# Kernel optimization log

Hardware: AMD Instinct MI355X
Metric: run time of the kernel (lower is better)

## Reference

```python
import jax, jax.numpy as jnp
import numpy as np

B = 256      # number of graphs
IN = 128     # input_dim
FD = 256     # feature_dim (dims[1])
HID = 256    # hidden_dim of attention block (dims[2])
OUT = 128    # final output dim (dims[3])
TXT = 512    # text_emb_dim

LENGTHS = np.asarray(128 + (np.arange(B) % 256), dtype=np.int64)  # ragged lens 128..383
N = int(LENGTHS.sum())  # 65408 total nodes
LMAX = int(LENGTHS.max())  # 383


def setup_inputs() -> dict:
    key = jax.random.key(0)
    ks = jax.random.split(key, 16)
    s = 0.02
    return {
        "input": jax.random.normal(ks[0], (N, IN), jnp.float32),
        "text_emb": jax.random.normal(ks[1], (B, TXT), jnp.float32),
        "repeat_list": jnp.asarray(LENGTHS),
        # layer 0: Linear(IN -> FD)
        "W0": jax.random.normal(ks[2], (IN, FD), jnp.float32) * s,
        "b0": jax.random.normal(ks[3], (FD,), jnp.float32) * s,
        # cross-attention block params
        "Wq": jax.random.normal(ks[4], (TXT, FD), jnp.float32) * s,
        "bq": jax.random.normal(ks[5], (FD,), jnp.float32) * s,
        "Wk": jax.random.normal(ks[6], (FD, FD), jnp.float32) * s,
        "bk": jax.random.normal(ks[7], (FD,), jnp.float32) * s,
        "Wv": jax.random.normal(ks[8], (FD, FD), jnp.float32) * s,
        "bv": jax.random.normal(ks[9], (FD,), jnp.float32) * s,
        "Wo": jax.random.normal(ks[10], (FD, HID), jnp.float32) * s,
        "bo": jax.random.normal(ks[11], (HID,), jnp.float32) * s,
        # layer 2: Linear(HID -> OUT), last layer (no activation)
        "W2": jax.random.normal(ks[12], (HID, OUT), jnp.float32) * s,
        "b2": jax.random.normal(ks[13], (OUT,), jnp.float32) * s,
    }


def _cross_attention(h, text_emb, repeat_list, Wq, bq, Wk, bk, Wv, bv, Wo, bo):
    # h: [N, FD] packed ragged node features; repeat_list: [B] lengths (constant ints)
    n = h.shape[0]
    b = repeat_list.shape[0]
    fd = h.shape[1]
    # pad ragged -> [B, LMAX, FD] (pad value 0) + validity mask
    seg = jnp.repeat(jnp.arange(b), repeat_list, total_repeat_length=n)  # [N] graph id
    offsets = jnp.cumsum(repeat_list) - repeat_list                      # [B] start of each graph
    pos = jnp.arange(n) - offsets[seg]                                   # [N] within-graph pos
    padded = jnp.zeros((b, LMAX, fd), h.dtype).at[seg, pos].set(h)
    valid = jnp.arange(LMAX)[None, :] < repeat_list[:, None]             # [B, L]

    q = text_emb @ Wq + bq                              # [B, FD]
    k = (padded @ Wk + bk) * valid[..., None]           # masked_fill(mask==0, 0)
    v = (padded @ Wv + bv) * valid[..., None]

    # query is broadcast identically over the padded-length axis, so each row of the
    # [L, L] score matrix is the same vector: scores[b, j] = q[b] . k[b, j]
    scores = jnp.einsum('bf,bjf->bj', q, k)             # [B, L]
    scores = jnp.where(valid, scores, -jnp.inf)         # mask invalid columns j
    p = jax.nn.softmax(scores, axis=-1)                 # [B, L]
    # output = attention^T @ value with identical rows => out[b,j,:] = p[b,j] * sum_i v[b,i,:]
    v_sum = v.sum(axis=1)                               # [B, FD] (padded rows already zero)
    out_pad = p[..., None] * v_sum[:, None, :]          # [B, L, FD]
    out_nodes = out_pad[seg, pos]                       # unpad-concat -> [N, FD]
    return out_nodes @ Wo + bo                          # [N, HID]


def reference(input, text_emb, repeat_list, W0, b0, Wq, bq, Wk, bk, Wv, bv, Wo, bo, W2, b2):
    h = jax.nn.relu(input @ W0 + b0)                                     # layer 0 + relu
    h = _cross_attention(h, text_emb, repeat_list, Wq, bq, Wk, bk, Wv, bv, Wo, bo)
    h = jax.nn.relu(h)                                                   # layer 1 + relu
    return h @ W2 + b2                                                   # layer 2 (last, no act)
```

## Files before the change

### kernel.cpp

```cpp
#include <hip/hip_runtime.h>
#include <math.h>

#define B_G   256
#define IN_D  128
#define FD    256
#define HID   256
#define OUT_D 128
#define TXT   512
#define XKS   136

typedef short bf16x8 __attribute__((ext_vector_type(8)));
typedef float f32x4  __attribute__((ext_vector_type(4)));

__device__ __forceinline__ unsigned bf_rne(float x) {
    unsigned u = __float_as_uint(x);
    u += 0x7fffu + ((u >> 16) & 1u);
    return u >> 16;
}
__device__ __forceinline__ float bf_to_f(unsigned h) {
    return __uint_as_float(h << 16);
}
__device__ __forceinline__ void split2(float a0, float a1, unsigned& hp, unsigned& lp) {
    unsigned h0 = bf_rne(a0), h1 = bf_rne(a1);
    float r0 = a0 - bf_to_f(h0), r1 = a1 - bf_to_f(h1);
    hp = h0 | (h1 << 16);
    lp = bf_rne(r0) | (bf_rne(r1) << 16);
}

__global__ __launch_bounds__(256) void k_prepA(
    const float* __restrict__ text_emb, const float* __restrict__ Wq,
    const float* __restrict__ bq, const float* __restrict__ Wk,
    const float* __restrict__ W0, const int* __restrict__ lens,
    float* __restrict__ qk, int* __restrict__ offsets, float* __restrict__ hsum,
    unsigned short* __restrict__ W0sH, unsigned short* __restrict__ W0sL)
{
    int blk = blockIdx.x, t = threadIdx.x;
    __shared__ float te[TXT];
    __shared__ float q[FD];
    __shared__ int   sc[B_G];

    if (blk < 256) {
        int b = blk;
        hsum[b * FD + t] = 0.f;
        for (int i = t; i < TXT; i += 256) te[i] = text_emb[(size_t)b * TXT + i];
        __syncthreads();
        float acc = bq[t];
        for (int k = 0; k < TXT; k++) acc = fmaf(te[k], Wq[k * FD + t], acc);
        q[t] = acc;
        __syncthreads();
        float a2 = 0.f;
        for (int f = 0; f < FD; f++) a2 = fmaf(Wk[t * FD + f], q[f], a2);
        qk[b * FD + t] = a2;
    } else if (blk < 260) {
        int e = (blk - 256) * 256 + t;
        int kc = e >> 8, c = e & 255;
        size_t base = (size_t)(kc * 256 + c) * 32;
        for (int kk = 0; kk < 32; kk++) {
            float v = W0[(size_t)(kc * 32 + kk) * FD + c];
            unsigned h = bf_rne(v);
            float r = v - bf_to_f(h);
            W0sH[base + kk] = (unsigned short)h;
            W0sL[base + kk] = (unsigned short)bf_rne(r);
        }
    } else {
        sc[t] = lens[t];
        __syncthreads();
        for (int d = 1; d < 256; d <<= 1) {
            int v = (t >= d) ? sc[t - d] : 0;
            __syncthreads();
            sc[t] += v;
            __syncthreads();
        }
        offsets[t + 1] = sc[t];
        if (t == 0) offsets[0] = 0;
    }
}

__global__ __launch_bounds__(256, 4) void k_l0_mfma(
    const float* __restrict__ X,
    const unsigned short* __restrict__ W0sH, const unsigned short* __restrict__ W0sL,
    const float* __restrict__ b0, const float* __restrict__ qk,
    const int* __restrict__ offsets,
    float* __restrict__ scores, float* __restrict__ hsum)
{
    int b = blockIdx.y;
    int off = offsets[b], len = offsets[b + 1] - off;
    int n0 = blockIdx.x * 64;
    if (n0 >= len) return;
    int nvalid = min(64, len - n0);

    __shared__ __align__(16) unsigned short XsH[64 * XKS], XsL[64 * XKS];
    __shared__ float qks[FD];
    __shared__ float bsh[FD];
    __shared__ float red[4][64];

    int tid = threadIdx.x;
    int lane = tid & 63, w = tid >> 6;
    int ln = lane & 15, quad = lane >> 4;

    qks[tid] = qk[b * FD + tid];
    bsh[tid] = b0[tid];

    {
        int node_s = tid >> 2, ks = (tid & 3) * 32;
        const float4* Xr4 = (const float4*)(X + (size_t)(off + n0 + node_s) * IN_D + ks);
        bool v = (node_s < nvalid);
#pragma unroll
        for (int g = 0; g < 4; g++) {
            float4 a, c4;
            if (v) { a = Xr4[2 * g]; c4 = Xr4[2 * g + 1]; }
            else   { a = make_float4(0.f, 0.f, 0.f, 0.f); c4 = a; }
            uint4 hq, lq;
            split2(a.x,  a.y,  hq.x, lq.x);
            split2(a.z,  a.w,  hq.y, lq.y);
            split2(c4.x, c4.y, hq.z, lq.z);
            split2(c4.z, c4.w, hq.w, lq.w);
            *(uint4*)&XsH[node_s * XKS + ks + g * 8] = hq;
            *(uint4*)&XsL[node_s * XKS + ks + g * 8] = lq;
        }
    }
    __syncthreads();

    f32x4 acc[4][4] = {};
#pragma unroll
    for (int kc = 0; kc < 4; kc++) {
        bf16x8 AH[4], AL[4];
#pragma unroll
        for (int i = 0; i < 4; i++) {
            AH[i] = *(const bf16x8*)&XsH[(16 * i + ln) * XKS + kc * 32 + quad * 8];
            AL[i] = *(const bf16x8*)&XsL[(16 * i + ln) * XKS + kc * 32 + quad * 8];
        }
#pragma unroll
        for (int j = 0; j < 4; j++) {
            int c = 64 * w + 16 * j + ln;
            size_t base = (size_t)(kc * 256 + c) * 32 + quad * 8;
            bf16x8 BH = *(const bf16x8*)&W0sH[base];
            bf16x8 BL = *(const bf16x8*)&W0sL[base];
#pragma unroll
            for (int i = 0; i < 4; i++) {
                acc[i][j] = __builtin_amdgcn_mfma_f32_16x16x32_bf16(AH[i], BH, acc[i][j], 0, 0, 0);
                acc[i][j] = __builtin_amdgcn_mfma_f32_16x16x32_bf16(AH[i], BL, acc[i][j], 0, 0, 0);
                acc[i][j] = __builtin_amdgcn_mfma_f32_16x16x32_bf16(AL[i], BH, acc[i][j], 0, 0, 0);
            }
        }
    }

    float sp[4][4];
    float cs[4] = {0.f, 0.f, 0.f, 0.f};
#pragma unroll
    for (int i = 0; i < 4; i++)
#pragma unroll
        for (int r = 0; r < 4; r++) sp[i][r] = 0.f;

#pragma unroll
    for (int i = 0; i < 4; i++)
#pragma unroll
        for (int j = 0; j < 4; j++) {
            int c = 64 * w + 16 * j + ln;
            float bb = bsh[c], qv = qks[c];
#pragma unroll
            for (int r = 0; r < 4; r++) {
                int node = 16 * i + 4 * quad + r;
                float h = acc[i][j][r] + bb;
                h = (h > 0.f && node < nvalid) ? h : 0.f;
                sp[i][r] = fmaf(h, qv, sp[i][r]);
                cs[j] += h;
            }
        }
#pragma unroll
    for (int i = 0; i < 4; i++)
#pragma unroll
        for (int r = 0; r < 4; r++) {
            float s = sp[i][r];
            s += __shfl_xor(s, 1); s += __shfl_xor(s, 2);
            s += __shfl_xor(s, 4); s += __shfl_xor(s, 8);
            sp[i][r] = s;
        }
    if (ln == 0) {
#pragma unroll
        for (int i = 0; i < 4; i++)
#pragma unroll
            for (int r = 0; r < 4; r++)
                red[w][16 * i + 4 * quad + r] = sp[i][r];
    }
#pragma unroll
    for (int j = 0; j < 4; j++) {
        float s = cs[j];
        s += __shfl_xor(s, 16); s += __shfl_xor(s, 32);
        if (quad == 0) atomicAdd(&hsum[b * FD + 64 * w + 16 * j + ln], s);
    }
    __syncthreads();
    if (tid < 64 && tid < nvalid)
        scores[off + n0 + tid] = red[0][tid] + red[1][tid] + red[2][tid] + red[3][tid];
}

__global__ __launch_bounds__(1024) void k_graph_walk(
    const float* __restrict__ scores, const float* __restrict__ hsum,
    const float* __restrict__ Wv, const float* __restrict__ bv,
    const float* __restrict__ Wo, const float* __restrict__ bo,
    const float* __restrict__ W2, const float* __restrict__ b2,
    const int* __restrict__ offsets, float* __restrict__ Y)
{
    int b = blockIdx.x, tid = threadIdx.x;
    int off = offsets[b], len = offsets[b + 1] - off;
    int t = tid & 255, g = tid >> 8;

    __shared__ float redm[16], reds[16];
    __shared__ float hs[FD], vs[FD];
    __shared__ float part[4][FD];
    __shared__ float wv2[HID], boS[HID], b2s[OUT_D];
    __shared__ float tOrig[256];
    __shared__ float tS[256], dwS[256], dbS[256];
    __shared__ int   kS[256];
    __shared__ int   cnt[257], startS[257];
    __shared__ float A0s[OUT_D], C0s[OUT_D];
    __shared__ float segA[8][OUT_D], segC[8][OUT_D];
    __shared__ __align__(16) char ops_raw[656 * 16];
    float* opA = (float*)ops_raw;
    float* opB = (float*)(ops_raw + 2624);
    int*   opN = (int*)(ops_raw + 5248);
    int*   opK = (int*)(ops_raw + 7872);

    if (g == 0) { boS[t] = bo[t]; hs[t] = hsum[b * FD + t]; }
    if (tid < OUT_D) b2s[tid] = b2[tid];
    if (tid <= 256) cnt[tid] = 0;
    float s_n = (tid < len) ? scores[off + tid] : -INFINITY;

    float m = s_n;
#pragma unroll
    for (int d = 1; d < 64; d <<= 1) m = fmaxf(m, __shfl_xor(m, d));
    if ((tid & 63) == 0) redm[tid >> 6] = m;
    __syncthreads();
    m = -INFINITY;
#pragma unroll
    for (int k = 0; k < 16; k++) m = fmaxf(m, redm[k]);

    float e_n = (tid < len) ? expf(s_n - m) : 0.f;
    float s = e_n;
#pragma unroll
    for (int d = 1; d < 64; d <<= 1) s += __shfl_xor(s, d);
    if ((tid & 63) == 0) reds[tid >> 6] = s;
    __syncthreads();
    s = 0.f;
#pragma unroll
    for (int k = 0; k < 16; k++) s += reds[k];
    float dinv = 1.0f / s;

    float acc = (g == 0) ? (float)len * bv[t] : 0.f;
    for (int f = 64 * g; f < 64 * g + 64; f++) acc = fmaf(hs[f], Wv[f * FD + t], acc);
    part[g][t] = acc;
    __syncthreads();
    if (g == 0) vs[t] = part[0][t] + part[1][t] + part[2][t] + part[3][t];
    __syncthreads();
    float a2 = 0.f;
    for (int f = 64 * g; f < 64 * g + 64; f++) a2 = fmaf(vs[f], Wo[f * HID + t], a2);
    part[g][t] = a2;
    __syncthreads();
    if (g == 0) wv2[t] = part[0][t] + part[1][t] + part[2][t] + part[3][t];
    __syncthreads();

    bool real = false;
    if (tid < 256) {
        float wv = wv2[tid], bvv = boS[tid];
        bool isev = (wv > 0.f && bvv < 0.f) || (wv < 0.f && bvv > 0.f);
        float tk = isev ? (-bvv / wv) : INFINITY;
        real = isev && (tk < INFINITY);
        tOrig[tid] = real ? tk : INFINITY;
    }
    __syncthreads();

    if (tid < 256) {
        float tk = tOrig[tid];
        int r = 0;
        for (int j = 0; j < 256; j++) {
            float tj = tOrig[j];
            r += (tj < tk || (tj == tk && j < tid)) ? 1 : 0;
        }
        tS[r] = tk;
        kS[r] = tid;
        float wv = wv2[tid], bvv = boS[tid];
        dwS[r] = real ? fabsf(wv) : 0.f;
        dbS[r] = real ? -fabsf(bvv) : 0.f;
    }
    {
        int q = tid >> 7, c = tid & 127;
        float pa = 0.f, pc = 0.f;
        for (int k = q * 32; k < q * 32 + 32; ++k) {
            float v = W2[(size_t)k * OUT_D + c];
            float wv = wv2[k], bvv = boS[k];
            bool ini = (bvv > 0.f) || (bvv == 0.f && wv > 0.f);
            pa = fmaf(ini ? wv : 0.f, v, pa);
            pc = fmaf(ini ? bvv : 0.f, v, pc);
        }
        segA[q][c] = pa; segC[q][c] = pc;
    }
    int nE = __syncthreads_count(real);

    float p_n = 0.f; int r_n = 0;
    if (tid < len) {
        p_n = e_n * dinv;
        int r = 0;
#pragma unroll
        for (int st = 128; st > 0; st >>= 1)
            if (tS[r + st - 1] < p_n) r += st;
        r_n = r;
        atomicAdd(&cnt[r], 1);
    }
    if (tid < OUT_D) {
        float sa = 0.f, sc2 = 0.f;
#pragma unroll
        for (int q = 0; q < 8; q++) { sa += segA[q][tid]; sc2 += segC[q][tid]; }
        A0s[tid] = sa; C0s[tid] = sc2;
    }
    __syncthreads();

    if (tid < 64) {
        int l = tid;
        int v0 = cnt[4 * l], v1 = cnt[4 * l + 1], v2 = cnt[4 * l + 2], v3 = cnt[4 * l + 3];
        int s0 = v0, s1 = s0 + v1, s2 = s1 + v2, s3 = s2 + v3;
        int run = s3;
#pragma unroll
        for (int d = 1; d < 64; d <<= 1) {
            int t2 = __shfl_up(run, d);
            if (l >= d) run += t2;
        }
        int base = run - s3;
        startS[4 * l + 0] = base;      cnt[4 * l + 0] = base;
        startS[4 * l + 1] = base + s0; cnt[4 * l + 1] = base + s0;
        startS[4 * l + 2] = base + s1; cnt[4 * l + 2] = base + s1;
        startS[4 * l + 3] = base + s2; cnt[4 * l + 3] = base + s2;
        if (l == 63) { startS[256] = base + s3; cnt[256] = base + s3; }
    }
    __syncthreads();

    int L    = len + nE;
    int Lpad = (L + 7) & ~7;
    int Lseg = ((Lpad + 63) >> 6) << 3;

    if (tid < len) {
        int slot = atomicAdd(&cnt[r_n], 1);
        int pos = slot + r_n;
        opA[pos] = p_n; opB[pos] = 0.f; opN[pos] = tid; opK[pos] = 0;
    }
    if (tid < nE) {
        int pos = startS[tid + 1] + tid;
        opA[pos] = dwS[tid]; opB[pos] = dbS[tid]; opN[pos] = -1; opK[pos] = kS[tid];
    }
    for (int i = L + tid; i < 648; i += 1024) {
        opA[i] = 0.f; opB[i] = 0.f; opN[i] = -1; opK[i] = 0;
    }
    __syncthreads();

    int sg = tid >> 7, c = tid & 127;
    {
        int iBeg = sg * Lseg, iEnd = iBeg + Lseg;
        int lo = 0, hi = nE;
        while (lo < hi) {
            int mid = (lo + hi) >> 1;
            if (startS[mid + 1] + mid < iBeg) lo = mid + 1; else hi = mid;
        }
        float dA = 0.f, dC = 0.f;
        for (int j = lo; j < nE && (startS[j + 1] + j) < iEnd; ++j) {
            float v = W2[(size_t)kS[j] * OUT_D + c];
            dA = fmaf(dwS[j], v, dA);
            dC = fmaf(dbS[j], v, dC);
        }
        segA[sg][c] = dA; segC[sg][c] = dC;
    }
    __syncthreads();

    {
        float A = A0s[c], C = C0s[c];
        for (int s2 = 0; s2 < sg; ++s2) { A += segA[s2][c]; C += segC[s2][c]; }
        float b2v = b2s[c];
        float* Yb = Y + (size_t)off * OUT_D + c;
        int i0 = sg * Lseg;

        float rA[8], rB[8], rV[8] = {0,0,0,0,0,0,0,0};
        int rN[8], rK[8];
#pragma unroll
        for (int u = 0; u < 8; ++u) {
            rA[u] = opA[i0 + u]; rB[u] = opB[i0 + u];
            rN[u] = opN[i0 + u]; rK[u] = opK[i0 + u];
        }
#pragma unroll
        for (int u = 0; u < 8; ++u)
            if (rN[u] < 0) rV[u] = W2[(size_t)rK[u] * OUT_D + c];

        for (int i0w = i0; i0w < i0 + Lseg; i0w += 8) {
#pragma unroll
            for (int u = 0; u < 8; ++u) {
                int i = i0w + u;
                float aI = rA[u], bI = rB[u], vv = rV[u];
                int nI = rN[u];
                rA[u] = opA[i + 8]; rB[u] = opB[i + 8];
                rN[u] = opN[i + 8]; rK[u] = opK[i + 8];
                if (rN[u] < 0) rV[u] = W2[(size_t)rK[u] * OUT_D + c];
                if (nI >= 0) Yb[(size_t)nI * OUT_D] = fmaf(aI, A, C) + b2v;
                else { A = fmaf(aI, vv, A); C = fmaf(bI, vv, C); }
            }
        }
    }
}

extern "C" void kernel_launch(void* const* d_in, const int* in_sizes, int n_in,
                              void* d_out, int out_size, void* d_ws, size_t ws_size,
                              hipStream_t stream)
{
    const float* X        = (const float*)d_in[0];
    const float* text_emb = (const float*)d_in[1];
    const int*   lens     = (const int*)d_in[2];
    const float* W0       = (const float*)d_in[3];
    const float* b0       = (const float*)d_in[4];
    const float* Wq       = (const float*)d_in[5];
    const float* bq       = (const float*)d_in[6];
    const float* Wk       = (const float*)d_in[7];
    const float* Wv       = (const float*)d_in[9];
    const float* bv       = (const float*)d_in[10];
    const float* Wo       = (const float*)d_in[11];
    const float* bo       = (const float*)d_in[12];
    const float* W2       = (const float*)d_in[13];
    const float* b2       = (const float*)d_in[14];
    float* Y = (float*)d_out;

    char* base = (char*)d_ws;
    size_t o = 0;
    int*   offsets = (int*)(base + o);            o += 1088;
    float* qkbuf   = (float*)(base + o);          o += 262144;
    float* hsum    = (float*)(base + o);          o += 262144;
    float* scores  = (float*)(base + o);          o += 262144;
    unsigned short* W0sH = (unsigned short*)(base + o); o += 65536;
    unsigned short* W0sL = (unsigned short*)(base + o); o += 65536;

    k_prepA<<<261, 256, 0, stream>>>(text_emb, Wq, bq, Wk, W0, lens,
                                     qkbuf, offsets, hsum, W0sH, W0sL);
    k_l0_mfma<<<dim3(6, B_G), 256, 0, stream>>>(X, W0sH, W0sL, b0, qkbuf, offsets, scores, hsum);
    k_graph_walk<<<B_G, 1024, 0, stream>>>(scores, hsum, Wv, bv, Wo, bo, W2, b2, offsets, Y);
}
```

Before: 215.8 us.

## Pack graph-walk ops into int4 and broadcast them across the wave with readlane

The four separate LDS op arrays become one int4 array of records. Each wave loads its segment's records once, one per lane, into registers. Per-step operands are then broadcast with readlane instead of every thread re-reading LDS. The event-prefix pass now scans this register-resident list and drops the binary search over startS, and the rank computation reads tOrig as float4. This cuts LDS load traffic and latency in the serial walk, at the cost of more scalar readlane instructions and relying on segments fitting in two 64-entry register windows.

New measurement: 205.0 us. 5.0% less time.

```diff
diff --git a/kernel.cpp b/kernel.cpp
--- a/kernel.cpp
+++ b/kernel.cpp
@@ -204,22 +204,19 @@
     int b = blockIdx.x, tid = threadIdx.x;
     int off = offsets[b], len = offsets[b + 1] - off;
     int t = tid & 255, g = tid >> 8;
+    int lane = tid & 63;
 
     __shared__ float redm[16], reds[16];
     __shared__ float hs[FD], vs[FD];
     __shared__ float part[4][FD];
     __shared__ float wv2[HID], boS[HID], b2s[OUT_D];
-    __shared__ float tOrig[256];
+    __shared__ __align__(16) float tOrig[256];
     __shared__ float tS[256], dwS[256], dbS[256];
     __shared__ int   kS[256];
     __shared__ int   cnt[257], startS[257];
     __shared__ float A0s[OUT_D], C0s[OUT_D];
     __shared__ float segA[8][OUT_D], segC[8][OUT_D];
-    __shared__ __align__(16) char ops_raw[656 * 16];
-    float* opA = (float*)ops_raw;
-    float* opB = (float*)(ops_raw + 2624);
-    int*   opN = (int*)(ops_raw + 5248);
-    int*   opK = (int*)(ops_raw + 7872);
+    __shared__ __align__(16) int4 ops4[704];
 
     if (g == 0) { boS[t] = bo[t]; hs[t] = hsum[b * FD + t]; }
     if (tid < OUT_D) b2s[tid] = b2[tid];
@@ -272,9 +269,14 @@
     if (tid < 256) {
         float tk = tOrig[tid];
         int r = 0;
-        for (int j = 0; j < 256; j++) {
-            float tj = tOrig[j];
-            r += (tj < tk || (tj == tk && j < tid)) ? 1 : 0;
+        const float4* t4 = (const float4*)tOrig;
+        for (int j4 = 0; j4 < 64; ++j4) {
+            float4 tj = t4[j4];
+            int e0 = 4 * j4;
+            r += (tj.x < tk || (tj.x == tk && (e0 + 0) < tid)) ? 1 : 0;
+            r += (tj.y < tk || (tj.y == tk && (e0 + 1) < tid)) ? 1 : 0;
+            r += (tj.z < tk || (tj.z == tk && (e0 + 2) < tid)) ? 1 : 0;
+            r += (tj.w < tk || (tj.w == tk && (e0 + 3) < tid)) ? 1 : 0;
         }
         tS[r] = tk;
         kS[r] = tid;
@@ -336,34 +338,42 @@
     int L    = len + nE;
     int Lpad = (L + 7) & ~7;
     int Lseg = ((Lpad + 63) >> 6) << 3;
+    int sg = tid >> 7, c = tid & 127;
 
     if (tid < len) {
         int slot = atomicAdd(&cnt[r_n], 1);
         int pos = slot + r_n;
-        opA[pos] = p_n; opB[pos] = 0.f; opN[pos] = tid; opK[pos] = 0;
+        ops4[pos] = make_int4(__float_as_int(p_n), 0, tid, 0);
     }
     if (tid < nE) {
         int pos = startS[tid + 1] + tid;
-        opA[pos] = dwS[tid]; opB[pos] = dbS[tid]; opN[pos] = -1; opK[pos] = kS[tid];
-    }
-    for (int i = L + tid; i < 648; i += 1024) {
-        opA[i] = 0.f; opB[i] = 0.f; opN[i] = -1; opK[i] = 0;
-    }
-    __syncthreads();
-
-    int sg = tid >> 7, c = tid & 127;
+        ops4[pos] = make_int4(__float_as_int(dwS[tid]), __float_as_int(dbS[tid]), -1, kS[tid]);
+    }
+    for (int i = L + tid; i < 704; i += 1024)
+        ops4[i] = make_int4(0, 0, -1, 0);
+    __syncthreads();
+
+    int i0 = sg * Lseg;
+    int4 cur = ops4[i0 + lane];
+    int4 nxt = ops4[i0 + 64 + lane];
+
     {
-        int iBeg = sg * Lseg, iEnd = iBeg + Lseg;
-        int lo = 0, hi = nE;
-        while (lo < hi) {
-            int mid = (lo + hi) >> 1;
-            if (startS[mid + 1] + mid < iBeg) lo = mid + 1; else hi = mid;
-        }
         float dA = 0.f, dC = 0.f;
-        for (int j = lo; j < nE && (startS[j + 1] + j) < iEnd; ++j) {
-            float v = W2[(size_t)kS[j] * OUT_D + c];
-            dA = fmaf(dwS[j], v, dA);
-            dC = fmaf(dbS[j], v, dC);
+        for (int ii = 0; ii < Lseg; ii += 8) {
+            int4 rc = (ii < 64) ? cur : nxt;
+            int bb = ii & 63;
+#pragma unroll
+            for (int d = 0; d < 8; ++d) {
+                int nI = __builtin_amdgcn_readlane(rc.z, bb + d);
+                if (nI < 0) {
+                    float aI = __uint_as_float((unsigned)__builtin_amdgcn_readlane(rc.x, bb + d));
+                    float bI = __uint_as_float((unsigned)__builtin_amdgcn_readlane(rc.y, bb + d));
+                    int   kI = __builtin_amdgcn_readlane(rc.w, bb + d);
+                    float v = W2[(size_t)kI * OUT_D + c];
+                    dA = fmaf(aI, v, dA);
+                    dC = fmaf(bI, v, dC);
+                }
+            }
         }
         segA[sg][c] = dA; segC[sg][c] = dC;
     }
@@ -374,30 +384,35 @@
         for (int s2 = 0; s2 < sg; ++s2) { A += segA[s2][c]; C += segC[s2][c]; }
         float b2v = b2s[c];
         float* Yb = Y + (size_t)off * OUT_D + c;
-        int i0 = sg * Lseg;
-
-        float rA[8], rB[8], rV[8] = {0,0,0,0,0,0,0,0};
-        int rN[8], rK[8];
-#pragma unroll
-        for (int u = 0; u < 8; ++u) {
-            rA[u] = opA[i0 + u]; rB[u] = opB[i0 + u];
-            rN[u] = opN[i0 + u]; rK[u] = opK[i0 + u];
-        }
-#pragma unroll
-        for (int u = 0; u < 8; ++u)
-            if (rN[u] < 0) rV[u] = W2[(size_t)rK[u] * OUT_D + c];
-
-        for (int i0w = i0; i0w < i0 + Lseg; i0w += 8) {
-#pragma unroll
-            for (int u = 0; u < 8; ++u) {
-                int i = i0w + u;
-                float aI = rA[u], bI = rB[u], vv = rV[u];
-                int nI = rN[u];
-                rA[u] = opA[i + 8]; rB[u] = opB[i + 8];
-                rN[u] = opN[i + 8]; rK[u] = opK[i + 8];
-                if (rN[u] < 0) rV[u] = W2[(size_t)rK[u] * OUT_D + c];
-                if (nI >= 0) Yb[(size_t)nI * OUT_D] = fmaf(aI, A, C) + b2v;
-                else { A = fmaf(aI, vv, A); C = fmaf(bI, vv, C); }
+
+        float rV[8];
+#pragma unroll
+        for (int d = 0; d < 8; ++d) {
+            int nU = __builtin_amdgcn_readlane(cur.z, d);
+            int kU = __builtin_amdgcn_readlane(cur.w, d);
+            if (nU < 0) rV[d] = W2[(size_t)kU * OUT_D + c];
+            else        rV[d] = 0.f;
+        }
+        for (int ii = 0; ii < Lseg; ii += 8) {
+            int4 rc = (ii < 64) ? cur : nxt;
+            int bc = ii & 63;
+            int4 rp = (ii + 8 < 64) ? cur : nxt;
+            int bp = (ii + 8) & 63;
+#pragma unroll
+            for (int d = 0; d < 8; ++d) {
+                float aI = __uint_as_float((unsigned)__builtin_amdgcn_readlane(rc.x, bc + d));
+                int   nI = __builtin_amdgcn_readlane(rc.z, bc + d);
+                int   np = __builtin_amdgcn_readlane(rp.z, bp + d);
+                int   kp = __builtin_amdgcn_readlane(rp.w, bp + d);
+                float vv = rV[d];
+                if (nI >= 0) {
+                    Yb[(size_t)nI * OUT_D] = fmaf(aI, A, C) + b2v;
+                } else {
+                    float bI = __uint_as_float((unsigned)__builtin_amdgcn_readlane(rc.y, bc + d));
+                    A = fmaf(aI, vv, A);
+                    C = fmaf(bI, vv, C);
+                }
+                if (np < 0) rV[d] = W2[(size_t)kp * OUT_D + c];
             }
         }
     }
```
